# Kernel optimization log

Hardware: AMD Instinct MI355X
Metric: run time of the kernel (lower is better)

The kernel has to match this reference:

```python
import jax, jax.numpy as jnp
import numpy as np

B, C, H, W, KS = 64, 128, 36, 100, 9
WSCALE = 0.02  # < 1/sqrt(C*KS) to keep the additive recurrence stable


def setup_inputs() -> dict:
    key = jax.random.key(0)
    kx, kd, ku, kr, kl = jax.random.split(key, 5)
    return {
        "x": jax.random.normal(kx, (B, C, H, W), dtype=jnp.float32),
        "w_d": jax.random.normal(kd, (C, C, KS), dtype=jnp.float32) * WSCALE,
        "w_u": jax.random.normal(ku, (C, C, KS), dtype=jnp.float32) * WSCALE,
        "w_r": jax.random.normal(kr, (C, C, KS), dtype=jnp.float32) * WSCALE,
        "w_l": jax.random.normal(kl, (C, C, KS), dtype=jnp.float32) * WSCALE,
    }


def _conv1d(z, w):
    # z: [B, C, L], w: [Cout, Cin, ks], SAME padding (matches padding=ks//2, bias=False)
    ks = w.shape[-1]
    return jax.lax.conv_general_dilated(
        z, w, window_strides=(1,), padding=[(ks // 2, ks // 2)],
        dimension_numbers=("NCH", "OIH", "NCH"))


def _scan_dir(x, w, axis, reverse):
    # singleDURL: out[0] = slice[0]; out[i] = slice[i] + relu(conv(out[i-1]))
    xs = jnp.moveaxis(x, axis, 0)  # [L, B, C, M]
    if reverse:
        xs = xs[::-1]

    def step(carry, s):
        nxt = s + jax.nn.relu(_conv1d(carry, w))
        return nxt, nxt

    _, outs = jax.lax.scan(step, xs[0], xs[1:])
    outs = jnp.concatenate([xs[:1], outs], axis=0)
    if reverse:
        outs = outs[::-1]
    return jnp.moveaxis(outs, 0, axis)


def reference(x, w_d, w_u, w_r, w_l):
    # allDURL: D (down, scan over H, 1xks conv over W), U (up), R (right, scan over W,
    # ksx1 conv over H), L (left)
    x = _scan_dir(x, w_d, axis=2, reverse=False)
    x = _scan_dir(x, w_u, axis=2, reverse=True)
    x = _scan_dir(x, w_r, axis=3, reverse=False)
    x = _scan_dir(x, w_l, axis=3, reverse=True)
    return x
```

## Files before the change

### kernel.cpp

```cpp
#include <hip/hip_runtime.h>

#define Bn 64
#define Cn 128
#define Hn 36
#define Wn 100
#define KSn 9

#define B_STRIDE (Cn * Hn * Wn)
#define C_STRIDE (Hn * Wn)

#define WH_CHUNK 80
#define WW_CHUNK 40
#define WH_SIZE (16 * Cn * WH_CHUNK)
#define WW_SIZE (32 * Cn * WW_CHUNK)

__global__ void __launch_bounds__(256) k_copy(const float4* __restrict__ s,
                                              float4* __restrict__ d, int n4) {
  int i = blockIdx.x * 256 + threadIdx.x;
  if (i < n4) d[i] = s[i];
}

__global__ void __launch_bounds__(256) k_zero(unsigned* p, int n) {
  int i = blockIdx.x * 256 + threadIdx.x;
  if (i < n) p[i] = 0u;
}

__global__ void __launch_bounds__(256) k_prep_h(const float* __restrict__ w,
                                                float* __restrict__ o) {
  int i = blockIdx.x * 256 + threadIdx.x;
  if (i >= 16 * Cn * 72) return;
  int k = i % 9, j = (i / 9) % 8, ci = (i / 72) % Cn, cog = i / (72 * Cn);
  o[(cog * Cn + ci) * WH_CHUNK + j * 9 + k] = w[((cog * 8 + j) * Cn + ci) * KSn + k];
}
__global__ void __launch_bounds__(256) k_prep_w(const float* __restrict__ w,
                                                float* __restrict__ o) {
  int i = blockIdx.x * 256 + threadIdx.x;
  if (i >= 32 * Cn * 36) return;
  int k = i % 9, j = (i / 9) % 4, ci = (i / 36) % Cn, coq = i / (36 * Cn);
  o[(coq * Cn + ci) * WW_CHUNK + j * 9 + k] = w[((coq * 4 + j) * Cn + ci) * KSn + k];
}

__device__ __forceinline__ void bbar(unsigned* c, unsigned target) {
  __syncthreads();
  if (threadIdx.x == 0) {
    __hip_atomic_fetch_add(c, 1u, __ATOMIC_RELEASE, __HIP_MEMORY_SCOPE_AGENT);
    while (__hip_atomic_load(c, __ATOMIC_RELAXED, __HIP_MEMORY_SCOPE_AGENT) <
           target)
      __builtin_amdgcn_s_sleep(1);
    __builtin_amdgcn_fence(__ATOMIC_ACQUIRE, "agent");
  }
  __syncthreads();
}

__global__ void __launch_bounds__(512, 1) k_hfused(float* __restrict__ buf,
                                                   const float* __restrict__ pwd,
                                                   const float* __restrict__ pwu,
                                                   unsigned* __restrict__ ctr) {
  __shared__ float prev[Cn][Wn + 8];
  const int bid = blockIdx.x;
  const int b = bid & 63;
  const int coq = bid >> 6;
  const int t = threadIdx.x;
  const int w = t & 127;
  const int plane = __builtin_amdgcn_readfirstlane(t >> 7);
  const int cog = coq * 4 + plane;
  unsigned* myc = ctr + b;
  unsigned gen = 0;

  for (int phase = 0; phase < 2; ++phase) {
    const float* wp = phase ? pwu : pwd;
    const float* wb = wp + (size_t)cog * Cn * WH_CHUNK;
    for (int s = 0; s < Hn - 1; ++s) {
      const int hc = phase ? (Hn - 2 - s) : (1 + s);
      const int hp = phase ? (hc + 1) : (hc - 1);

      const float* rb = buf + ((size_t)b * Cn * Hn + hp) * Wn;
      for (int g = t; g < Cn * 25; g += 512) {
        int ci = g / 25, wq = g % 25;
        *(float4*)&prev[ci][4 + wq * 4] =
            *(const float4*)(rb + (size_t)ci * C_STRIDE + wq * 4);
      }
      for (int g = t; g < Cn * 8; g += 512) {
        int ci = g >> 3, sp = g & 7;
        prev[ci][(sp < 4) ? sp : (Wn + sp)] = 0.f;
      }
      __syncthreads();

      if (w < Wn) {
        float acc[8] = {0.f, 0.f, 0.f, 0.f, 0.f, 0.f, 0.f, 0.f};
#pragma unroll 2
        for (int ci = 0; ci < Cn; ++ci) {
          float p[KSn];
#pragma unroll
          for (int k = 0; k < KSn; ++k) p[k] = prev[ci][w + k];
          const float* wr = wb + ci * WH_CHUNK;
#pragma unroll
          for (int j = 0; j < 8; ++j)
#pragma unroll
            for (int k = 0; k < KSn; ++k) acc[j] = fmaf(p[k], wr[j * 9 + k], acc[j]);
        }
        float* ob = buf + ((size_t)(b * Cn + cog * 8) * Hn + hc) * Wn + w;
#pragma unroll
        for (int j = 0; j < 8; ++j) ob[(size_t)j * C_STRIDE] += fmaxf(acc[j], 0.f);
      }
      ++gen;
      bbar(myc, gen * 4u);
    }
  }
}

__global__ void __launch_bounds__(512, 1) k_wfused(float* __restrict__ tb,
                                                   const float* __restrict__ pwr,
                                                   const float* __restrict__ pwl,
                                                   unsigned* __restrict__ ctr) {
  __shared__ float prev[Cn][Hn + 8];
  const int bid = blockIdx.x;
  const int b = bid & 63;
  const int coq = bid >> 6;
  const int t = threadIdx.x;
  const int h = t & 63;
  const int v = __builtin_amdgcn_readfirstlane(t >> 6);
  const int quadg = coq * 8 + v;
  unsigned* myc = ctr + b;
  unsigned gen = 0;

  for (int phase = 0; phase < 2; ++phase) {
    const float* wp = phase ? pwl : pwr;
    const float* wb = wp + (size_t)quadg * Cn * WW_CHUNK;
    for (int s = 0; s < Wn - 1; ++s) {
      const int wc = phase ? (Wn - 2 - s) : (1 + s);
      const int wpos = phase ? (wc + 1) : (wc - 1);

      const float* cb = tb + ((size_t)b * Cn * Wn + wpos) * Hn;
      for (int g = t; g < Cn * 9; g += 512) {
        int ci = g / 9, hq = g % 9;
        *(float4*)&prev[ci][4 + hq * 4] =
            *(const float4*)(cb + (size_t)ci * C_STRIDE + hq * 4);
      }
      for (int g = t; g < Cn * 8; g += 512) {
        int ci = g >> 3, sp = g & 7;
        prev[ci][(sp < 4) ? sp : (Hn + sp)] = 0.f;
      }
      __syncthreads();

      if (h < Hn) {
        float acc[4] = {0.f, 0.f, 0.f, 0.f};
#pragma unroll 2
        for (int ci = 0; ci < Cn; ++ci) {
          float p[KSn];
#pragma unroll
          for (int k = 0; k < KSn; ++k) p[k] = prev[ci][h + k];
          const float* wr = wb + ci * WW_CHUNK;
#pragma unroll
          for (int j = 0; j < 4; ++j)
#pragma unroll
            for (int k = 0; k < KSn; ++k) acc[j] = fmaf(p[k], wr[j * 9 + k], acc[j]);
        }
        float* ob = tb + ((size_t)(b * Cn + quadg * 4) * Wn + wc) * Hn + h;
#pragma unroll
        for (int j = 0; j < 4; ++j) ob[(size_t)j * C_STRIDE] += fmaxf(acc[j], 0.f);
      }
      ++gen;
      bbar(myc, gen * 4u);
    }
  }
}

__global__ void __launch_bounds__(256) k_t_hw2wh(const float* __restrict__ in,
                                                 float* __restrict__ out) {
  __shared__ float tile[Hn][Wn + 1];
  const int bc = blockIdx.x;
  const float* ib = in + (size_t)bc * C_STRIDE;
  float* ob = out + (size_t)bc * C_STRIDE;
  for (int f = threadIdx.x; f < Hn * Wn; f += 256) tile[f / Wn][f % Wn] = ib[f];
  __syncthreads();
  for (int f = threadIdx.x; f < Hn * Wn; f += 256) {
    int w = f / Hn, hh = f % Hn;
    ob[f] = tile[hh][w];
  }
}
__global__ void __launch_bounds__(256) k_t_wh2hw(const float* __restrict__ in,
                                                 float* __restrict__ out) {
  __shared__ float tile[Hn][Wn + 1];
  const int bc = blockIdx.x;
  const float* ib = in + (size_t)bc * C_STRIDE;
  float* ob = out + (size_t)bc * C_STRIDE;
  for (int f = threadIdx.x; f < Hn * Wn; f += 256) {
    int w = f / Hn, hh = f % Hn;
    tile[hh][w] = ib[f];
  }
  __syncthreads();
  for (int f = threadIdx.x; f < Hn * Wn; f += 256) ob[f] = tile[f / Wn][f % Wn];
}

__global__ void __launch_bounds__(128) k_hstep(float* __restrict__ buf,
                                               const float* __restrict__ wt,
                                               int hp, int hc) {
  __shared__ float prev[Cn][Wn + 8];
  const int b = blockIdx.x;
  const int cog = blockIdx.y;
  const int t = threadIdx.x;
  const float* rb = buf + ((size_t)b * Cn * Hn + hp) * Wn;
  for (int g = t; g < Cn * (Wn / 4); g += 128) {
    int ci = g / 25, wq = g % 25;
    float4 vv = *(const float4*)(rb + (size_t)ci * C_STRIDE + wq * 4);
    *(float4*)&prev[ci][4 + wq * 4] = vv;
  }
  for (int g = t; g < Cn * 8; g += 128) {
    int ci = g >> 3, s = g & 7;
    prev[ci][(s < 4) ? s : (Wn + s)] = 0.f;
  }
  __syncthreads();
  if (t >= Wn) return;
  float acc[8] = {0.f, 0.f, 0.f, 0.f, 0.f, 0.f, 0.f, 0.f};
  const float* wb = wt + (size_t)cog * 8 * Cn * KSn;
  for (int ci = 0; ci < Cn; ++ci) {
    float p[KSn];
#pragma unroll
    for (int k = 0; k < KSn; ++k) p[k] = prev[ci][t + k];
#pragma unroll
    for (int j = 0; j < 8; ++j) {
      const float* w9 = wb + ((size_t)j * Cn + ci) * KSn;
#pragma unroll
      for (int k = 0; k < KSn; ++k) acc[j] = fmaf(p[k], w9[k], acc[j]);
    }
  }
  float* ob = buf + ((size_t)(b * Cn + cog * 8) * Hn + hc) * Wn + t;
#pragma unroll
  for (int j = 0; j < 8; ++j) ob[(size_t)j * C_STRIDE] += fmaxf(acc[j], 0.f);
}
__global__ void __launch_bounds__(128) k_wstep_d(float* __restrict__ buf,
                                                 const float* __restrict__ wt,
                                                 int wpos, int wc) {
  __shared__ float prev[Cn][Hn + 8];
  const int b = blockIdx.x;
  const int cog = blockIdx.y;
  const int t = threadIdx.x;
  const int h = t & 63;
  const int jb = __builtin_amdgcn_readfirstlane((t >> 6) * 4);
  for (int g = t; g < Cn * Hn; g += 128) {
    int ci = g / Hn, hh = g % Hn;
    prev[ci][4 + hh] = buf[((size_t)(b * Cn + ci) * Hn + hh) * Wn + wpos];
  }
  for (int g = t; g < Cn * 8; g += 128) {
    int ci = g >> 3, s = g & 7;
    prev[ci][(s < 4) ? s : (Hn + s)] = 0.f;
  }
  __syncthreads();
  if (h >= Hn) return;
  float acc[4] = {0.f, 0.f, 0.f, 0.f};
  const float* wb = wt + (size_t)(cog * 8 + jb) * Cn * KSn;
  for (int ci = 0; ci < Cn; ++ci) {
    float p[KSn];
#pragma unroll
    for (int k = 0; k < KSn; ++k) p[k] = prev[ci][h + k];
#pragma unroll
    for (int j = 0; j < 4; ++j) {
      const float* w9 = wb + ((size_t)j * Cn + ci) * KSn;
#pragma unroll
      for (int k = 0; k < KSn; ++k) acc[j] = fmaf(p[k], w9[k], acc[j]);
    }
  }
  float* ob = buf + ((size_t)(b * Cn + cog * 8 + jb) * Hn + h) * Wn + wc;
#pragma unroll
  for (int j = 0; j < 4; ++j) ob[(size_t)j * C_STRIDE] += fmaxf(acc[j], 0.f);
}

extern "C" void kernel_launch(void* const* d_in, const int* in_sizes, int n_in,
                              void* d_out, int out_size, void* d_ws, size_t ws_size,
                              hipStream_t stream) {
  (void)in_sizes; (void)n_in; (void)out_size;
  const float* x  = (const float*)d_in[0];
  const float* wd = (const float*)d_in[1];
  const float* wu = (const float*)d_in[2];
  const float* wr = (const float*)d_in[3];
  const float* wl = (const float*)d_in[4];
  float* buf = (float*)d_out;
  const size_t nelem = (size_t)Bn * B_STRIDE;
  const size_t need = (nelem + 2 * (size_t)WH_SIZE + 2 * (size_t)WW_SIZE) * 4 + 512;

  k_copy<<<(int)(nelem / 4 + 255) / 256, 256, 0, stream>>>(
      (const float4*)x, (float4*)buf, (int)(nelem / 4));

  if (ws_size >= need) {
    float* tb  = (float*)d_ws;
    float* pwd = tb + nelem;
    float* pwu = pwd + WH_SIZE;
    float* pwr = pwu + WH_SIZE;
    float* pwl = pwr + WW_SIZE;
    unsigned* ctr = (unsigned*)(pwl + WW_SIZE);

    k_zero<<<1, 256, 0, stream>>>(ctr, 128);
    k_prep_h<<<(16 * Cn * 72 + 255) / 256, 256, 0, stream>>>(wd, pwd);
    k_prep_h<<<(16 * Cn * 72 + 255) / 256, 256, 0, stream>>>(wu, pwu);
    k_prep_w<<<(32 * Cn * 36 + 255) / 256, 256, 0, stream>>>(wr, pwr);
    k_prep_w<<<(32 * Cn * 36 + 255) / 256, 256, 0, stream>>>(wl, pwl);

    k_hfused<<<256, 512, 0, stream>>>(buf, pwd, pwu, ctr);
    k_t_hw2wh<<<Bn * Cn, 256, 0, stream>>>(buf, tb);
    k_wfused<<<256, 512, 0, stream>>>(tb, pwr, pwl, ctr + 64);
    k_t_wh2hw<<<Bn * Cn, 256, 0, stream>>>(tb, buf);
  } else {
    dim3 g8(Bn, Cn / 8);
    for (int hh = 1; hh < Hn; ++hh)
      k_hstep<<<g8, 128, 0, stream>>>(buf, wd, hh - 1, hh);
    for (int hh = Hn - 2; hh >= 0; --hh)
      k_hstep<<<g8, 128, 0, stream>>>(buf, wu, hh + 1, hh);
    for (int ww = 1; ww < Wn; ++ww)
      k_wstep_d<<<g8, 128, 0, stream>>>(buf, wr, ww - 1, ww);
    for (int ww = Wn - 2; ww >= 0; --ww)
      k_wstep_d<<<g8, 128, 0, stream>>>(buf, wl, ww + 1, ww);
  }
}
```

Baseline: 11.54 ms.

## Use 1024-thread blocks with fewer output channels per wave and prefetched weights

The fused H and W scan kernels now run 1024-thread blocks. Each wave computes fewer output channels (4 instead of 8 for H, 2 instead of 4 for W), and the H kernel splits the width across two waves. Weights for the next input channel are loaded as float4 vectors into registers one channel ahead of use, and a zero VGPR offset forces vector loads in place of scalar loads. The aim is more active waves per CU to hide latency and better-pipelined weight fetches, at the cost of reloading the previous row more often per output and of higher register pressure.

After: 25.84 ms. 2.24x slower.

```diff
diff --git a/kernel.cpp b/kernel.cpp
--- a/kernel.cpp
+++ b/kernel.cpp
@@ -9,10 +9,10 @@
 #define B_STRIDE (Cn * Hn * Wn)
 #define C_STRIDE (Hn * Wn)
 
-#define WH_CHUNK 80
-#define WW_CHUNK 40
-#define WH_SIZE (16 * Cn * WH_CHUNK)
-#define WW_SIZE (32 * Cn * WW_CHUNK)
+#define WQ_CHUNK 40
+#define WP_CHUNK 20
+#define WQ_SIZE (32 * Cn * WQ_CHUNK)
+#define WP_SIZE (64 * Cn * WP_CHUNK)
 
 __global__ void __launch_bounds__(256) k_copy(const float4* __restrict__ s,
                                               float4* __restrict__ d, int n4) {
@@ -25,19 +25,19 @@
   if (i < n) p[i] = 0u;
 }
 
-__global__ void __launch_bounds__(256) k_prep_h(const float* __restrict__ w,
-                                                float* __restrict__ o) {
-  int i = blockIdx.x * 256 + threadIdx.x;
-  if (i >= 16 * Cn * 72) return;
-  int k = i % 9, j = (i / 9) % 8, ci = (i / 72) % Cn, cog = i / (72 * Cn);
-  o[(cog * Cn + ci) * WH_CHUNK + j * 9 + k] = w[((cog * 8 + j) * Cn + ci) * KSn + k];
-}
-__global__ void __launch_bounds__(256) k_prep_w(const float* __restrict__ w,
+__global__ void __launch_bounds__(256) k_prep_q(const float* __restrict__ w,
                                                 float* __restrict__ o) {
   int i = blockIdx.x * 256 + threadIdx.x;
   if (i >= 32 * Cn * 36) return;
   int k = i % 9, j = (i / 9) % 4, ci = (i / 36) % Cn, coq = i / (36 * Cn);
-  o[(coq * Cn + ci) * WW_CHUNK + j * 9 + k] = w[((coq * 4 + j) * Cn + ci) * KSn + k];
+  o[(coq * Cn + ci) * WQ_CHUNK + j * 9 + k] = w[((coq * 4 + j) * Cn + ci) * KSn + k];
+}
+__global__ void __launch_bounds__(256) k_prep_p(const float* __restrict__ w,
+                                                float* __restrict__ o) {
+  int i = blockIdx.x * 256 + threadIdx.x;
+  if (i >= 64 * Cn * 18) return;
+  int k = i % 9, j = (i / 9) % 2, ci = (i / 18) % Cn, cop = i / (18 * Cn);
+  o[(cop * Cn + ci) * WP_CHUNK + j * 9 + k] = w[((cop * 2 + j) * Cn + ci) * KSn + k];
 }
 
 __device__ __forceinline__ void bbar(unsigned* c, unsigned target) {
@@ -52,56 +52,83 @@
   __syncthreads();
 }
 
-__global__ void __launch_bounds__(512, 1) k_hfused(float* __restrict__ buf,
-                                                   const float* __restrict__ pwd,
-                                                   const float* __restrict__ pwu,
-                                                   unsigned* __restrict__ ctr) {
+template <int NCO>
+__device__ __forceinline__ void fma_taps(const float4* q, const float* pp,
+                                         float* acc) {
+#pragma unroll
+  for (int j = 0; j < NCO; ++j)
+#pragma unroll
+    for (int k = 0; k < KSn; ++k) {
+      const int d = j * 9 + k;
+      const float wv = ((d & 3) == 0)   ? q[d >> 2].x
+                       : ((d & 3) == 1) ? q[d >> 2].y
+                       : ((d & 3) == 2) ? q[d >> 2].z
+                                        : q[d >> 2].w;
+      acc[j] = fmaf(pp[k], wv, acc[j]);
+    }
+}
+
+__global__ void __launch_bounds__(1024, 1) k_hfused3(float* __restrict__ buf,
+                                                     const float* __restrict__ pwd,
+                                                     const float* __restrict__ pwu,
+                                                     unsigned* __restrict__ ctr) {
   __shared__ float prev[Cn][Wn + 8];
-  const int bid = blockIdx.x;
-  const int b = bid & 63;
-  const int coq = bid >> 6;
-  const int t = threadIdx.x;
-  const int w = t & 127;
-  const int plane = __builtin_amdgcn_readfirstlane(t >> 7);
-  const int cog = coq * 4 + plane;
+  const int b = blockIdx.x, cg = blockIdx.y, t = threadIdx.x;
+  const int lane = t & 63;
+  const int v = __builtin_amdgcn_readfirstlane(t >> 6);
+  const int quad = v >> 1, wh = v & 1;
+  const int coqg = cg * 8 + quad;
+  const int w = wh * 50 + lane;
+  int vz;
+  asm volatile("v_mov_b32 %0, 0" : "=v"(vz));
   unsigned* myc = ctr + b;
   unsigned gen = 0;
 
   for (int phase = 0; phase < 2; ++phase) {
-    const float* wp = phase ? pwu : pwd;
-    const float* wb = wp + (size_t)cog * Cn * WH_CHUNK;
+    const float* wsel = phase ? pwu : pwd;
+    const float* wb = wsel + (size_t)coqg * Cn * WQ_CHUNK + vz;
     for (int s = 0; s < Hn - 1; ++s) {
       const int hc = phase ? (Hn - 2 - s) : (1 + s);
       const int hp = phase ? (hc + 1) : (hc - 1);
 
       const float* rb = buf + ((size_t)b * Cn * Hn + hp) * Wn;
-      for (int g = t; g < Cn * 25; g += 512) {
+      for (int g = t; g < Cn * 25; g += 1024) {
         int ci = g / 25, wq = g % 25;
         *(float4*)&prev[ci][4 + wq * 4] =
             *(const float4*)(rb + (size_t)ci * C_STRIDE + wq * 4);
       }
-      for (int g = t; g < Cn * 8; g += 512) {
+      for (int g = t; g < Cn * 8; g += 1024) {
         int ci = g >> 3, sp = g & 7;
         prev[ci][(sp < 4) ? sp : (Wn + sp)] = 0.f;
       }
       __syncthreads();
 
-      if (w < Wn) {
-        float acc[8] = {0.f, 0.f, 0.f, 0.f, 0.f, 0.f, 0.f, 0.f};
-#pragma unroll 2
-        for (int ci = 0; ci < Cn; ++ci) {
-          float p[KSn];
-#pragma unroll
-          for (int k = 0; k < KSn; ++k) p[k] = prev[ci][w + k];
-          const float* wr = wb + ci * WH_CHUNK;
-#pragma unroll
-          for (int j = 0; j < 8; ++j)
-#pragma unroll
-            for (int k = 0; k < KSn; ++k) acc[j] = fmaf(p[k], wr[j * 9 + k], acc[j]);
+      if (lane < 50) {
+        float acc[4] = {0.f, 0.f, 0.f, 0.f};
+        float4 qa[9], qb[9];
+#pragma unroll
+        for (int r = 0; r < 9; ++r) qa[r] = ((const float4*)wb)[r];
+#pragma unroll 1
+        for (int ci = 0; ci < Cn; ci += 2) {
+          const float4* n1 = (const float4*)(wb + (ci + 1) * WQ_CHUNK);
+#pragma unroll
+          for (int r = 0; r < 9; ++r) qb[r] = n1[r];
+          float pp[9];
+#pragma unroll
+          for (int k = 0; k < KSn; ++k) pp[k] = prev[ci][w + k];
+          fma_taps<4>(qa, pp, acc);
+          if (ci + 2 < Cn) {
+            const float4* n2 = (const float4*)(wb + (ci + 2) * WQ_CHUNK);
+#pragma unroll
+            for (int r = 0; r < 9; ++r) qa[r] = n2[r];
+          }
+#pragma unroll
+          for (int k = 0; k < KSn; ++k) pp[k] = prev[ci + 1][w + k];
+          fma_taps<4>(qb, pp, acc);
         }
-        float* ob = buf + ((size_t)(b * Cn + cog * 8) * Hn + hc) * Wn + w;
-#pragma unroll
-        for (int j = 0; j < 8; ++j) ob[(size_t)j * C_STRIDE] += fmaxf(acc[j], 0.f);
+        float* ob = buf + ((size_t)(b * Cn + coqg * 4) * Hn + hc) * Wn + w;
+#pragma unroll
+        for (int j = 0; j < 4; ++j) ob[(size_t)j * C_STRIDE] += fmaxf(acc[j], 0.f);
       }
       ++gen;
       bbar(myc, gen * 4u);
@@ -109,56 +136,65 @@
   }
 }
 
-__global__ void __launch_bounds__(512, 1) k_wfused(float* __restrict__ tb,
-                                                   const float* __restrict__ pwr,
-                                                   const float* __restrict__ pwl,
-                                                   unsigned* __restrict__ ctr) {
+__global__ void __launch_bounds__(1024, 1) k_wfused3(float* __restrict__ tb,
+                                                     const float* __restrict__ pwr,
+                                                     const float* __restrict__ pwl,
+                                                     unsigned* __restrict__ ctr) {
   __shared__ float prev[Cn][Hn + 8];
-  const int bid = blockIdx.x;
-  const int b = bid & 63;
-  const int coq = bid >> 6;
-  const int t = threadIdx.x;
-  const int h = t & 63;
+  const int b = blockIdx.x, cg = blockIdx.y, t = threadIdx.x;
+  const int lane = t & 63;
   const int v = __builtin_amdgcn_readfirstlane(t >> 6);
-  const int quadg = coq * 8 + v;
+  const int cop = cg * 16 + v;
+  int vz;
+  asm volatile("v_mov_b32 %0, 0" : "=v"(vz));
   unsigned* myc = ctr + b;
   unsigned gen = 0;
 
   for (int phase = 0; phase < 2; ++phase) {
-    const float* wp = phase ? pwl : pwr;
-    const float* wb = wp + (size_t)quadg * Cn * WW_CHUNK;
+    const float* wsel = phase ? pwl : pwr;
+    const float* wb = wsel + (size_t)cop * Cn * WP_CHUNK + vz;
     for (int s = 0; s < Wn - 1; ++s) {
       const int wc = phase ? (Wn - 2 - s) : (1 + s);
       const int wpos = phase ? (wc + 1) : (wc - 1);
 
       const float* cb = tb + ((size_t)b * Cn * Wn + wpos) * Hn;
-      for (int g = t; g < Cn * 9; g += 512) {
+      for (int g = t; g < Cn * 9; g += 1024) {
         int ci = g / 9, hq = g % 9;
         *(float4*)&prev[ci][4 + hq * 4] =
             *(const float4*)(cb + (size_t)ci * C_STRIDE + hq * 4);
       }
-      for (int g = t; g < Cn * 8; g += 512) {
+      for (int g = t; g < Cn * 8; g += 1024) {
         int ci = g >> 3, sp = g & 7;
         prev[ci][(sp < 4) ? sp : (Hn + sp)] = 0.f;
       }
       __syncthreads();
 
-      if (h < Hn) {
-        float acc[4] = {0.f, 0.f, 0.f, 0.f};
-#pragma unroll 2
-        for (int ci = 0; ci < Cn; ++ci) {
-          float p[KSn];
-#pragma unroll
-          for (int k = 0; k < KSn; ++k) p[k] = prev[ci][h + k];
-          const float* wr = wb + ci * WW_CHUNK;
-#pragma unroll
-          for (int j = 0; j < 4; ++j)
-#pragma unroll
-            for (int k = 0; k < KSn; ++k) acc[j] = fmaf(p[k], wr[j * 9 + k], acc[j]);
+      if (lane < Hn) {
+        float acc[2] = {0.f, 0.f};
+        float4 qa[5], qb[5];
+#pragma unroll
+        for (int r = 0; r < 5; ++r) qa[r] = ((const float4*)wb)[r];
+#pragma unroll 1
+        for (int ci = 0; ci < Cn; ci += 2) {
+          const float4* n1 = (const float4*)(wb + (ci + 1) * WP_CHUNK);
+#pragma unroll
+          for (int r = 0; r < 5; ++r) qb[r] = n1[r];
+          float pp[9];
+#pragma unroll
+          for (int k = 0; k < KSn; ++k) pp[k] = prev[ci][lane + k];
+          fma_taps<2>(qa, pp, acc);
+          if (ci + 2 < Cn) {
+            const float4* n2 = (const float4*)(wb + (ci + 2) * WP_CHUNK);
+#pragma unroll
+            for (int r = 0; r < 5; ++r) qa[r] = n2[r];
+          }
+#pragma unroll
+          for (int k = 0; k < KSn; ++k) pp[k] = prev[ci + 1][lane + k];
+          fma_taps<2>(qb, pp, acc);
         }
-        float* ob = tb + ((size_t)(b * Cn + quadg * 4) * Wn + wc) * Hn + h;
-#pragma unroll
-        for (int j = 0; j < 4; ++j) ob[(size_t)j * C_STRIDE] += fmaxf(acc[j], 0.f);
+        float* ob = tb + ((size_t)(b * Cn + cop * 2) * Wn + wc) * Hn + lane;
+        ob[0] += fmaxf(acc[0], 0.f);
+        ob[C_STRIDE] += fmaxf(acc[1], 0.f);
       }
       ++gen;
       bbar(myc, gen * 4u);
@@ -207,8 +243,8 @@
     *(float4*)&prev[ci][4 + wq * 4] = vv;
   }
   for (int g = t; g < Cn * 8; g += 128) {
-    int ci = g >> 3, s = g & 7;
-    prev[ci][(s < 4) ? s : (Wn + s)] = 0.f;
+    int ci = g >> 3, sp = g & 7;
+    prev[ci][(sp < 4) ? sp : (Wn + sp)] = 0.f;
   }
   __syncthreads();
   if (t >= Wn) return;
@@ -243,8 +279,8 @@
     prev[ci][4 + hh] = buf[((size_t)(b * Cn + ci) * Hn + hh) * Wn + wpos];
   }
   for (int g = t; g < Cn * 8; g += 128) {
-    int ci = g >> 3, s = g & 7;
-    prev[ci][(s < 4) ? s : (Hn + s)] = 0.f;
+    int ci = g >> 3, sp = g & 7;
+    prev[ci][(sp < 4) ? sp : (Hn + sp)] = 0.f;
   }
   __syncthreads();
   if (h >= Hn) return;
@@ -277,7 +313,8 @@
   const float* wl = (const float*)d_in[4];
   float* buf = (float*)d_out;
   const size_t nelem = (size_t)Bn * B_STRIDE;
-  const size_t need = (nelem + 2 * (size_t)WH_SIZE + 2 * (size_t)WW_SIZE) * 4 + 512;
+  const size_t need =
+      (nelem + 2 * (size_t)WQ_SIZE + 2 * (size_t)WP_SIZE) * 4 + 512;
 
   k_copy<<<(int)(nelem / 4 + 255) / 256, 256, 0, stream>>>(
       (const float4*)x, (float4*)buf, (int)(nelem / 4));
@@ -285,20 +322,21 @@
   if (ws_size >= need) {
     float* tb  = (float*)d_ws;
     float* pwd = tb + nelem;
-    float* pwu = pwd + WH_SIZE;
-    float* pwr = pwu + WH_SIZE;
-    float* pwl = pwr + WW_SIZE;
-    unsigned* ctr = (unsigned*)(pwl + WW_SIZE);
+    float* pwu = pwd + WQ_SIZE;
+    float* pwr = pwu + WQ_SIZE;
+    float* pwl = pwr + WP_SIZE;
+    unsigned* ctr = (unsigned*)(pwl + WP_SIZE);
 
     k_zero<<<1, 256, 0, stream>>>(ctr, 128);
-    k_prep_h<<<(16 * Cn * 72 + 255) / 256, 256, 0, stream>>>(wd, pwd);
-    k_prep_h<<<(16 * Cn * 72 + 255) / 256, 256, 0, stream>>>(wu, pwu);
-    k_prep_w<<<(32 * Cn * 36 + 255) / 256, 256, 0, stream>>>(wr, pwr);
-    k_prep_w<<<(32 * Cn * 36 + 255) / 256, 256, 0, stream>>>(wl, pwl);
-
-    k_hfused<<<256, 512, 0, stream>>>(buf, pwd, pwu, ctr);
+    k_prep_q<<<(32 * Cn * 36 + 255) / 256, 256, 0, stream>>>(wd, pwd);
+    k_prep_q<<<(32 * Cn * 36 + 255) / 256, 256, 0, stream>>>(wu, pwu);
+    k_prep_p<<<(64 * Cn * 18 + 255) / 256, 256, 0, stream>>>(wr, pwr);
+    k_prep_p<<<(64 * Cn * 18 + 255) / 256, 256, 0, stream>>>(wl, pwl);
+
+    dim3 g4(Bn, 4);
+    k_hfused3<<<g4, 1024, 0, stream>>>(buf, pwd, pwu, ctr);
     k_t_hw2wh<<<Bn * Cn, 256, 0, stream>>>(buf, tb);
-    k_wfused<<<256, 512, 0, stream>>>(tb, pwr, pwl, ctr + 64);
+    k_wfused3<<<g4, 1024, 0, stream>>>(tb, pwr, pwl, ctr + 64);
     k_t_wh2hw<<<Bn * Cn, 256, 0, stream>>>(tb, buf);
   } else {
     dim3 g8(Bn, Cn / 8);
```
